# Kernel tuning notes

Measured on AMD Instinct MI355X. Metric: run time of the kernel, lower is better.

## Reference

```python
import jax, jax.numpy as jnp
import numpy as np

N_NODES = 50000
N_EDGES = 800000
DIM_IN = 64
DIM_HID = 128
DIM_OUT = 64


def _linear_init(key, fan_in, fan_out):
    # torch nn.Linear default: U(-1/sqrt(fan_in), 1/sqrt(fan_in)) for W and b
    kw, kb = jax.random.split(key)
    bound = 1.0 / np.sqrt(fan_in)
    W = jax.random.uniform(kw, (fan_in, fan_out), minval=-bound, maxval=bound, dtype=jnp.float32)
    b = jax.random.uniform(kb, (fan_out,), minval=-bound, maxval=bound, dtype=jnp.float32)
    return W, b


def setup_inputs() -> dict:
    key = jax.random.key(0)
    kx, ke, k0, k1, k2 = jax.random.split(key, 5)
    x = jax.random.normal(kx, (N_NODES, DIM_IN), dtype=jnp.float32)
    edge_idx = jax.random.randint(ke, (2, N_EDGES), 0, N_NODES, dtype=jnp.int64)
    W0, b0 = _linear_init(k0, 2 * DIM_IN, DIM_HID)
    W1, b1 = _linear_init(k1, DIM_HID, DIM_HID)
    W2, b2 = _linear_init(k2, DIM_HID, DIM_OUT)
    return {"x": x, "edge_idx": edge_idx, "W0": W0, "b0": b0,
            "W1": W1, "b1": b1, "W2": W2, "b2": b2}


def reference(x, edge_idx, W0, b0, W1, b1, W2, b2):
    row, col = edge_idx[0], edge_idx[1]
    # gather + concat edge features: [E, 2*dim_in]
    h = jnp.concatenate([x[row], x[col]], axis=-1)
    h = jax.nn.softplus(h @ W0 + b0)
    h = jax.nn.softplus(h @ W1 + b1)
    h = h @ W2 + b2  # [E, dim_out]
    # scatter-add edge messages to source nodes
    return jax.ops.segment_sum(h, row, num_segments=x.shape[0])
```

## Files before the change

### kernel.cpp

```cpp
#include <hip/hip_runtime.h>
#include <math.h>

#define N_NODES 50000
#define N_EDGES 800000
#define DIM_IN 64
#define DIM_HID 128
#define DIM_OUT 64
#define PAD 136

typedef __attribute__((ext_vector_type(8))) short short8;
typedef __attribute__((ext_vector_type(4))) float f32x4;

union U8 { uint4 u; short8 s; };

__device__ __forceinline__ unsigned short f2bf(float f) {
    unsigned u = __float_as_uint(f);
    return (unsigned short)((u + 0x7fffu + ((u >> 16) & 1u)) >> 16);
}

__device__ __forceinline__ unsigned cvt_pk_bf16(float a, float b) {
    unsigned d;
    asm("v_cvt_pk_bf16_f32 %0, %1, %2" : "=v"(d) : "v"(a), "v"(b));
    return d;
}

__device__ __forceinline__ float exp2_fast(float a) {
#if __has_builtin(__builtin_amdgcn_exp2f)
    return __builtin_amdgcn_exp2f(a);
#else
    return __expf(a * 0.69314718f);
#endif
}

__device__ __forceinline__ unsigned sp2(float x0, float x1) {
    const float L2E = 1.44269504f;
    float z0 = exp2_fast(-fabsf(x0) * L2E);
    float z1 = exp2_fast(-fabsf(x1) * L2E);
    float p0 = fmaf(fmaf(fmaf(-0.1011458f, z0, 0.2942925f), z0, -0.5f), z0, 1.0f) * z0;
    float p1 = fmaf(fmaf(fmaf(-0.1011458f, z1, 0.2942925f), z1, -0.5f), z1, 1.0f) * z1;
    return cvt_pk_bf16(fmaxf(x0, 0.0f) + p0, fmaxf(x1, 0.0f) + p1);
}

__global__ void prep_all(const float* __restrict__ x,
                         const float* __restrict__ W0,
                         const float* __restrict__ W1,
                         const float* __restrict__ W2,
                         unsigned short* __restrict__ wt,
                         unsigned short* __restrict__ xbf,
                         float4* __restrict__ outz) {
    int i = blockIdx.x * blockDim.x + threadIdx.x;

    if (i < (N_NODES * DIM_OUT / 4))
        outz[i] = make_float4(0.f, 0.f, 0.f, 0.f);

    if (i < (N_NODES * DIM_IN / 4)) {
        float4 v = *((const float4*)x + i);
        uint2 p;
        p.x = cvt_pk_bf16(v.x, v.y);
        p.y = cvt_pk_bf16(v.z, v.w);
        *((uint2*)xbf + i) = p;
    }

    if (i < 320 * PAD) {
        int row = i / PAD, s = i - row * PAD;
        float v = 0.f;
        if (s < 128) {
            int f = ((s >> 5) << 5) | (((s & 7) >> 2) << 4) | (((s >> 3) & 3) << 2) | (s & 3);
            if (row < 128)      v = W0[s * DIM_HID + row];
            else if (row < 256) v = W1[f * DIM_HID + (row - 128)];
            else                v = W2[f * DIM_OUT + (row - 256)];
        }
        wt[i] = f2bf(v);
    }
}

__global__ void prep_weights(const float* __restrict__ W0,
                             const float* __restrict__ W1,
                             const float* __restrict__ W2,
                             unsigned short* __restrict__ wt) {
    int i = blockIdx.x * blockDim.x + threadIdx.x;
    if (i >= 320 * PAD) return;
    int row = i / PAD, s = i - row * PAD;
    float v = 0.f;
    if (s < 128) {
        int f = ((s >> 5) << 5) | (((s & 7) >> 2) << 4) | (((s >> 3) & 3) << 2) | (s & 3);
        if (row < 128)      v = W0[s * DIM_HID + row];
        else if (row < 256) v = W1[f * DIM_HID + (row - 128)];
        else                v = W2[f * DIM_OUT + (row - 256)];
    }
    wt[i] = f2bf(v);
}

template <bool XB>
__global__ __launch_bounds__(256, 4)
void edge_mlp_mfma(const float* __restrict__ x,
                   const unsigned short* __restrict__ xbf,
                   const int* __restrict__ eidx,
                   const unsigned short* __restrict__ wt,
                   const float* __restrict__ b0,
                   const float* __restrict__ b1,
                   const float* __restrict__ b2,
                   float* __restrict__ out) {
    __shared__ unsigned short lw[128 * PAD];

    const int lane = threadIdx.x & 63;
    const int w    = threadIdx.x >> 6;
    const int l16  = lane & 15;
    const int q    = lane >> 4;
    const int e0w  = blockIdx.x * 128 + w * 32;

    int nodeR[2], nodeC[2];
#pragma unroll
    for (int m = 0; m < 2; ++m) {
        nodeR[m] = eidx[e0w + m * 16 + l16];
        nodeC[m] = eidx[N_EDGES + e0w + m * 16 + l16];
    }

    int ns[8];
#pragma unroll
    for (int m = 0; m < 2; ++m)
#pragma unroll
        for (int r = 0; r < 4; ++r)
            ns[m * 4 + r] = eidx[e0w + m * 16 + q * 4 + r];

    short8 hfr[2][4];
#pragma unroll
    for (int m = 0; m < 2; ++m)
#pragma unroll
        for (int kk = 0; kk < 4; ++kk) {
            int node = (kk >= 2) ? nodeC[m] : nodeR[m];
            if (XB) {
                hfr[m][kk] = *(const short8*)(xbf + (size_t)node * DIM_IN + (kk & 1) * 32 + q * 8);
            } else {
                const float* p = x + (size_t)node * DIM_IN + (kk & 1) * 32 + q * 8;
                float4 v0 = *(const float4*)p;
                float4 v1 = *(const float4*)(p + 4);
                U8 t;
                t.u.x = cvt_pk_bf16(v0.x, v0.y);
                t.u.y = cvt_pk_bf16(v0.z, v0.w);
                t.u.z = cvt_pk_bf16(v1.x, v1.y);
                t.u.w = cvt_pk_bf16(v1.z, v1.w);
                hfr[m][kk] = t.s;
            }
        }

    {
        const uint4* src = (const uint4*)wt;
        uint4* dst = (uint4*)lw;
        for (int i = threadIdx.x; i < 2176; i += 256) dst[i] = src[i];
    }
    __syncthreads();

#pragma unroll
    for (int L = 0; L < 2; ++L) {
        const float* bias = L ? b1 : b0;
        unsigned d[2][8][2];
#pragma unroll
        for (int ti = 0; ti < 8; ++ti) {
            f32x4 bb = *(const f32x4*)(bias + ti * 16 + q * 4);
            f32x4 a0 = bb, a1 = bb;
            const unsigned short* Wp = lw + (ti * 16 + l16) * PAD + q * 8;
            short8 wf[4];
#pragma unroll
            for (int kk = 0; kk < 4; ++kk)
                wf[kk] = *(const short8*)(Wp + kk * 32);
#pragma unroll
            for (int kk = 0; kk < 4; ++kk) {
                a0 = __builtin_amdgcn_mfma_f32_16x16x32_bf16(wf[kk], hfr[0][kk], a0, 0, 0, 0);
                a1 = __builtin_amdgcn_mfma_f32_16x16x32_bf16(wf[kk], hfr[1][kk], a1, 0, 0, 0);
            }
            d[0][ti][0] = sp2(a0[0], a0[1]);
            d[0][ti][1] = sp2(a0[2], a0[3]);
            d[1][ti][0] = sp2(a1[0], a1[1]);
            d[1][ti][1] = sp2(a1[2], a1[3]);
        }
#pragma unroll
        for (int m = 0; m < 2; ++m)
#pragma unroll
            for (int kk = 0; kk < 4; ++kk) {
                U8 t;
                t.u.x = d[m][2 * kk][0];
                t.u.y = d[m][2 * kk][1];
                t.u.z = d[m][2 * kk + 1][0];
                t.u.w = d[m][2 * kk + 1][1];
                hfr[m][kk] = t.s;
            }
        __syncthreads();
        {
            const uint4* src = (const uint4*)(wt + (size_t)(L ? 256 : 128) * PAD);
            uint4* dst = (uint4*)lw;
            const int n = L ? 1088 : 2176;
            for (int i = threadIdx.x; i < n; i += 256) dst[i] = src[i];
        }
        __syncthreads();
    }

    {
        f32x4 acc[4][2];
#pragma unroll
        for (int ti = 0; ti < 4; ++ti) {
            float bv = b2[ti * 16 + l16];
            f32x4 a0 = (f32x4){bv, bv, bv, bv};
            f32x4 a1 = a0;
            const unsigned short* Wp = lw + (ti * 16 + l16) * PAD + q * 8;
            short8 wf[4];
#pragma unroll
            for (int kk = 0; kk < 4; ++kk)
                wf[kk] = *(const short8*)(Wp + kk * 32);
#pragma unroll
            for (int kk = 0; kk < 4; ++kk) {
                a0 = __builtin_amdgcn_mfma_f32_16x16x32_bf16(hfr[0][kk], wf[kk], a0, 0, 0, 0);
                a1 = __builtin_amdgcn_mfma_f32_16x16x32_bf16(hfr[1][kk], wf[kk], a1, 0, 0, 0);
            }
            acc[ti][0] = a0;
            acc[ti][1] = a1;
        }

#pragma unroll
        for (int ti = 0; ti < 4; ++ti)
#pragma unroll
            for (int r = 0; r < 4; ++r) {
                atomicAdd(out + (size_t)ns[r] * DIM_OUT + ti * 16 + l16, acc[ti][0][r]);
                atomicAdd(out + (size_t)ns[4 + r] * DIM_OUT + ti * 16 + l16, acc[ti][1][r]);
            }
    }
}

extern "C" void kernel_launch(void* const* d_in, const int* in_sizes, int n_in,
                              void* d_out, int out_size, void* d_ws, size_t ws_size,
                              hipStream_t stream) {
    const float* x  = (const float*)d_in[0];
    const int*   ei = (const int*)d_in[1];
    const float* W0 = (const float*)d_in[2];
    const float* b0 = (const float*)d_in[3];
    const float* W1 = (const float*)d_in[4];
    const float* b1 = (const float*)d_in[5];
    const float* W2 = (const float*)d_in[6];
    const float* b2 = (const float*)d_in[7];
    float* out = (float*)d_out;

    unsigned short* wt = (unsigned short*)d_ws;
    const size_t WT_BYTES = (size_t)320 * PAD * sizeof(unsigned short);
    unsigned short* xbf = (unsigned short*)((char*)d_ws + WT_BYTES);
    const size_t need = WT_BYTES + (size_t)N_NODES * DIM_IN * sizeof(unsigned short);

    if (ws_size >= need) {
        prep_all<<<(N_NODES * DIM_IN / 4 + 255) / 256, 256, 0, stream>>>(
            x, W0, W1, W2, wt, xbf, (float4*)out);
        edge_mlp_mfma<true><<<N_EDGES / 128, 256, 0, stream>>>(
            x, xbf, ei, wt, b0, b1, b2, out);
    } else {
        hipMemsetAsync(out, 0, (size_t)N_NODES * DIM_OUT * sizeof(float), stream);
        prep_weights<<<(320 * PAD + 255) / 256, 256, 0, stream>>>(W0, W1, W2, wt);
        edge_mlp_mfma<false><<<N_EDGES / 128, 256, 0, stream>>>(
            x, nullptr, ei, wt, b0, b1, b2, out);
    }
}
```

Measured before the change: 266.7 us.

## Halve LDS weight buffer to 64 rows and stream weights in halves

Shrinks the shared-memory weight tile from 128 to 64 rows so each hidden layer is processed in two halves, reloading the next 64-row chunk of weights between halves, and raises launch bounds to 8 blocks per CU. The goal is higher occupancy to hide gather latency in the edge MLP. In exchange it adds extra barriers and weight reloads per block, and the tighter launch bound may force register spills. Output zeroing moves from the prep kernel to a hipMemsetAsync, and the separate weight-prep kernel is merged into a templated prep_all.

```diff
diff --git a/kernel.cpp b/kernel.cpp
--- a/kernel.cpp
+++ b/kernel.cpp
@@ -41,19 +41,16 @@
     return cvt_pk_bf16(fmaxf(x0, 0.0f) + p0, fmaxf(x1, 0.0f) + p1);
 }
 
+template <bool DO_XBF>
 __global__ void prep_all(const float* __restrict__ x,
                          const float* __restrict__ W0,
                          const float* __restrict__ W1,
                          const float* __restrict__ W2,
                          unsigned short* __restrict__ wt,
-                         unsigned short* __restrict__ xbf,
-                         float4* __restrict__ outz) {
+                         unsigned short* __restrict__ xbf) {
     int i = blockIdx.x * blockDim.x + threadIdx.x;
 
-    if (i < (N_NODES * DIM_OUT / 4))
-        outz[i] = make_float4(0.f, 0.f, 0.f, 0.f);
-
-    if (i < (N_NODES * DIM_IN / 4)) {
+    if (DO_XBF && i < (N_NODES * DIM_IN / 4)) {
         float4 v = *((const float4*)x + i);
         uint2 p;
         p.x = cvt_pk_bf16(v.x, v.y);
@@ -74,25 +71,8 @@
     }
 }
 
-__global__ void prep_weights(const float* __restrict__ W0,
-                             const float* __restrict__ W1,
-                             const float* __restrict__ W2,
-                             unsigned short* __restrict__ wt) {
-    int i = blockIdx.x * blockDim.x + threadIdx.x;
-    if (i >= 320 * PAD) return;
-    int row = i / PAD, s = i - row * PAD;
-    float v = 0.f;
-    if (s < 128) {
-        int f = ((s >> 5) << 5) | (((s & 7) >> 2) << 4) | (((s >> 3) & 3) << 2) | (s & 3);
-        if (row < 128)      v = W0[s * DIM_HID + row];
-        else if (row < 256) v = W1[f * DIM_HID + (row - 128)];
-        else                v = W2[f * DIM_OUT + (row - 256)];
-    }
-    wt[i] = f2bf(v);
-}
-
 template <bool XB>
-__global__ __launch_bounds__(256, 4)
+__global__ __launch_bounds__(256, 8)
 void edge_mlp_mfma(const float* __restrict__ x,
                    const unsigned short* __restrict__ xbf,
                    const int* __restrict__ eidx,
@@ -101,7 +81,7 @@
                    const float* __restrict__ b1,
                    const float* __restrict__ b2,
                    float* __restrict__ out) {
-    __shared__ unsigned short lw[128 * PAD];
+    __shared__ unsigned short lw[64 * PAD];
 
     const int lane = threadIdx.x & 63;
     const int w    = threadIdx.x >> 6;
@@ -147,7 +127,11 @@
     {
         const uint4* src = (const uint4*)wt;
         uint4* dst = (uint4*)lw;
-        for (int i = threadIdx.x; i < 2176; i += 256) dst[i] = src[i];
+#pragma unroll
+        for (int it = 0; it < 5; ++it) {
+            int i = threadIdx.x + it * 256;
+            if (i < 1088) dst[i] = src[i];
+        }
     }
     __syncthreads();
 
@@ -156,23 +140,38 @@
         const float* bias = L ? b1 : b0;
         unsigned d[2][8][2];
 #pragma unroll
-        for (int ti = 0; ti < 8; ++ti) {
-            f32x4 bb = *(const f32x4*)(bias + ti * 16 + q * 4);
-            f32x4 a0 = bb, a1 = bb;
-            const unsigned short* Wp = lw + (ti * 16 + l16) * PAD + q * 8;
-            short8 wf[4];
-#pragma unroll
-            for (int kk = 0; kk < 4; ++kk)
-                wf[kk] = *(const short8*)(Wp + kk * 32);
-#pragma unroll
-            for (int kk = 0; kk < 4; ++kk) {
-                a0 = __builtin_amdgcn_mfma_f32_16x16x32_bf16(wf[kk], hfr[0][kk], a0, 0, 0, 0);
-                a1 = __builtin_amdgcn_mfma_f32_16x16x32_bf16(wf[kk], hfr[1][kk], a1, 0, 0, 0);
-            }
-            d[0][ti][0] = sp2(a0[0], a0[1]);
-            d[0][ti][1] = sp2(a0[2], a0[3]);
-            d[1][ti][0] = sp2(a1[0], a1[1]);
-            d[1][ti][1] = sp2(a1[2], a1[3]);
+        for (int half = 0; half < 2; ++half) {
+#pragma unroll
+            for (int ti = 0; ti < 4; ++ti) {
+                const int tiG = half * 4 + ti;
+                f32x4 bb = *(const f32x4*)(bias + tiG * 16 + q * 4);
+                f32x4 a0 = bb, a1 = bb;
+                const unsigned short* Wp = lw + (ti * 16 + l16) * PAD + q * 8;
+                short8 wf[4];
+#pragma unroll
+                for (int kk = 0; kk < 4; ++kk)
+                    wf[kk] = *(const short8*)(Wp + kk * 32);
+#pragma unroll
+                for (int kk = 0; kk < 4; ++kk) {
+                    a0 = __builtin_amdgcn_mfma_f32_16x16x32_bf16(wf[kk], hfr[0][kk], a0, 0, 0, 0);
+                    a1 = __builtin_amdgcn_mfma_f32_16x16x32_bf16(wf[kk], hfr[1][kk], a1, 0, 0, 0);
+                }
+                d[0][tiG][0] = sp2(a0[0], a0[1]);
+                d[0][tiG][1] = sp2(a0[2], a0[3]);
+                d[1][tiG][0] = sp2(a1[0], a1[1]);
+                d[1][tiG][1] = sp2(a1[2], a1[3]);
+            }
+            __syncthreads();
+            {
+                const uint4* src = (const uint4*)(wt + (size_t)(L * 2 + half + 1) * 64 * PAD);
+                uint4* dst = (uint4*)lw;
+#pragma unroll
+                for (int it = 0; it < 5; ++it) {
+                    int i = threadIdx.x + it * 256;
+                    if (i < 1088) dst[i] = src[i];
+                }
+            }
+            __syncthreads();
         }
 #pragma unroll
         for (int m = 0; m < 2; ++m)
@@ -185,14 +184,6 @@
                 t.u.w = d[m][2 * kk + 1][1];
                 hfr[m][kk] = t.s;
             }
-        __syncthreads();
-        {
-            const uint4* src = (const uint4*)(wt + (size_t)(L ? 256 : 128) * PAD);
-            uint4* dst = (uint4*)lw;
-            const int n = L ? 1088 : 2176;
-            for (int i = threadIdx.x; i < n; i += 256) dst[i] = src[i];
-        }
-        __syncthreads();
     }
 
     {
@@ -244,14 +235,16 @@
     unsigned short* xbf = (unsigned short*)((char*)d_ws + WT_BYTES);
     const size_t need = WT_BYTES + (size_t)N_NODES * DIM_IN * sizeof(unsigned short);
 
+    hipMemsetAsync(out, 0, (size_t)N_NODES * DIM_OUT * sizeof(float), stream);
+
     if (ws_size >= need) {
-        prep_all<<<(N_NODES * DIM_IN / 4 + 255) / 256, 256, 0, stream>>>(
-            x, W0, W1, W2, wt, xbf, (float4*)out);
+        prep_all<true><<<(N_NODES * DIM_IN / 4 + 255) / 256, 256, 0, stream>>>(
+            x, W0, W1, W2, wt, xbf);
         edge_mlp_mfma<true><<<N_EDGES / 128, 256, 0, stream>>>(
             x, xbf, ei, wt, b0, b1, b2, out);
     } else {
-        hipMemsetAsync(out, 0, (size_t)N_NODES * DIM_OUT * sizeof(float), stream);
-        prep_weights<<<(320 * PAD + 255) / 256, 256, 0, stream>>>(W0, W1, W2, wt);
+        prep_all<false><<<(320 * PAD + 255) / 256, 256, 0, stream>>>(
+            x, W0, W1, W2, wt, nullptr);
         edge_mlp_mfma<false><<<N_EDGES / 128, 256, 0, stream>>>(
             x, nullptr, ei, wt, b0, b1, b2, out);
     }
```

New measurement: 509.1 us. +90.9%, slower.
